# Kernel tuning notes

Measured on AMD Instinct MI355X. Metric: run time of the kernel, lower is better.

The kernel has to match this reference:

```python
import jax, jax.numpy as jnp
import numpy as np

N = 100000      # nodes
E = 1600000     # edges (avg degree 16)
F_IN = 64
HID = 128
OUT = 64


def setup_inputs() -> dict:
    key = jax.random.key(0)
    ks = jax.random.split(key, 12)
    s = lambda k, i, o: jax.random.normal(k, (i, o), jnp.float32) / np.sqrt(i)
    x = jax.random.normal(ks[0], (N, F_IN), jnp.float32)
    edge_index = jax.random.randint(ks[1], (2, E), 0, N, dtype=jnp.int64)
    return {
        "x": x,
        "edge_index": edge_index,
        # conv1: SAGEConv(F_IN -> HID): lin_l (neighbors, with bias), lin_r (root)
        "W1n": s(ks[2], F_IN, HID), "b1n": jnp.zeros((HID,), jnp.float32),
        "W1r": s(ks[3], F_IN, HID),
        # lin1: Linear(F_IN -> HID)
        "Wl1": s(ks[4], F_IN, HID), "bl1": jnp.zeros((HID,), jnp.float32),
        # conv2: SAGEConv(HID -> OUT)
        "W2n": s(ks[5], HID, OUT), "b2n": jnp.zeros((OUT,), jnp.float32),
        "W2r": s(ks[6], HID, OUT),
        # lin2: Linear(HID -> OUT)
        "Wl2": s(ks[7], HID, OUT), "bl2": jnp.zeros((OUT,), jnp.float32),
    }


def _sage(x, src, dst, Wn, bn, Wr):
    # mean aggregation of source-node features at destination nodes
    msg = x[src]                                             # [E, F]
    agg = jax.ops.segment_sum(msg, dst, num_segments=N)      # [N, F]
    deg = jax.ops.segment_sum(jnp.ones((src.shape[0],), x.dtype), dst,
                              num_segments=N)                # [N]
    mean = agg / jnp.maximum(deg, 1.0)[:, None]
    return mean @ Wn + bn + x @ Wr


def reference(x, edge_index, W1n, b1n, W1r, Wl1, bl1, W2n, b2n, W2r, Wl2, bl2):
    src, dst = edge_index[0], edge_index[1]
    h = _sage(x, src, dst, W1n, b1n, W1r) + (x @ Wl1 + bl1)
    h = jax.nn.relu(h)
    out = _sage(h, src, dst, W2n, b2n, W2r) + (h @ Wl2 + bl2)
    return out
```

## Files before the change

### kernel.cpp

```cpp
#include <hip/hip_runtime.h>


#define NN 100000
#define NE 1600000
#define SBW 256
#define NSB 391
#define CAP2 5120
#define EPB 6250
#define MB 256
#define BSB 256
#define W1B 32
#define W2B 32
#define XBLK ((NN * 8 + 511) / 512)

typedef __attribute__((ext_vector_type(8))) __bf16 bf16x8;
typedef __attribute__((ext_vector_type(4))) float f32x4;

__device__ __forceinline__ float b2f(unsigned short u) {
    unsigned v = ((unsigned)u) << 16;
    float f;
    __builtin_memcpy(&f, &v, 4);
    return f;
}
__device__ __forceinline__ float b2f_lo(unsigned v) {
    unsigned w = v << 16;
    float f;
    __builtin_memcpy(&f, &w, 4);
    return f;
}
__device__ __forceinline__ float b2f_hi(unsigned v) {
    unsigned w = v & 0xFFFF0000u;
    float f;
    __builtin_memcpy(&f, &w, 4);
    return f;
}
__device__ __forceinline__ unsigned short f2b(float f) {
    unsigned u;
    __builtin_memcpy(&u, &f, 4);
    u += 0x7FFFu + ((u >> 16) & 1u);
    return (unsigned short)(u >> 16);
}

__global__ __launch_bounds__(512) void front_kernel(
    const void* __restrict__ x, const int* __restrict__ ei,
    const void* W1n, const void* W1r, const void* Wl1,
    const void* b1n, const void* bl1,
    const void* W2n, const void* W2r, const void* Wl2,
    const void* b2n, const void* bl2,
    unsigned short* __restrict__ Wt1g, unsigned short* __restrict__ Wt2g,
    float* __restrict__ bias1, float* __restrict__ bias2,
    unsigned int* __restrict__ xbu,
    int* __restrict__ flags, int* __restrict__ cntP, int* __restrict__ ebuf) {
    __shared__ int lh[NSB];
    __shared__ int lbase[NSB];
    __shared__ int ldst[EPB];
    __shared__ int sred[256];
    int t = threadIdx.x;
    int b = blockIdx.x;

    if (b < BSB) {
        if (t < 256) sred[t] = ei[2 * t + 1];
        if (t < NSB) lh[t] = 0;
        __syncthreads();
        for (int s = 128; s > 0; s >>= 1) {
            if (t < s) sred[t] |= sred[t + s];
            __syncthreads();
        }
        bool i64 = (sred[0] == 0);
        int e0 = b * EPB;
        for (int i = t; i < EPB; i += 512) {
            int e = e0 + i;
            int d = i64 ? (int)((const long long*)ei)[NE + e] : ei[NE + e];
            ldst[i] = d;
            atomicAdd(&lh[d >> 8], 1);
        }
        __syncthreads();
        if (t < NSB) {
            int c = lh[t];
            lbase[t] = c ? atomicAdd(&cntP[t * 16], c) : 0;
            lh[t] = 0;
        }
        __syncthreads();
        for (int i = t; i < EPB; i += 512) {
            int e = e0 + i;
            int s = i64 ? (int)((const long long*)ei)[e] : ei[e];
            int d = ldst[i];
            int sb = d >> 8;
            int r = lbase[sb] + atomicAdd(&lh[sb], 1);
            if (r < CAP2) ebuf[sb * CAP2 + r] = (s << 8) | (d & 255);
        }
        return;
    }

    const unsigned int* xw = (const unsigned int*)x;
    if (t < 256) {
        unsigned e = (xw[t] >> 7) & 0xFFu;
        sred[t] = (e > 0x85u) ? 1 : 0;
    }
    __syncthreads();
    for (int s = 128; s > 0; s >>= 1) {
        if (t < s) sred[t] += sred[t + s];
        __syncthreads();
    }
    bool fp32 = sred[0] >= 32;
    auto rd = [&](const void* p, int i) -> float {
        return fp32 ? ((const float*)p)[i] : b2f(((const unsigned short*)p)[i]);
    };

    if (b < BSB + W1B) {
        int idx = (b - BSB) * 512 + t;
        int c = idx >> 7, k = idx & 127;
        float v = (k < 64) ? rd(W1n, k * 128 + c)
                           : rd(W1r, (k - 64) * 128 + c) + rd(Wl1, (k - 64) * 128 + c);
        Wt1g[c * 128 + k] = f2b(v);
        if (b == BSB) {
            if (t < 128) bias1[t] = rd(b1n, t) + rd(bl1, t);
            if (t == 0) flags[1] = fp32 ? 1 : 0;
        }
        return;
    }
    if (b < BSB + W1B + W2B) {
        int idx = (b - BSB - W1B) * 512 + t;
        int c = idx >> 7, k = idx & 127;
        float v = (c < 64) ? rd(W2n, k * 64 + c)
                           : rd(W2r, k * 64 + (c - 64)) + rd(Wl2, k * 64 + (c - 64));
        Wt2g[c * 128 + k] = f2b(v);
        if (b == BSB + W1B && t < 64) bias2[t] = rd(b2n, t) + rd(bl2, t);
        return;
    }
    int tt = (b - BSB - W1B - W2B) * 512 + t;
    if (tt >= NN * 8) return;
    if (fp32) {
        const float4* xf = (const float4*)x;
        float4 a = xf[2 * tt], c = xf[2 * tt + 1];
        uint4 o;
        o.x = f2b(a.x) | ((unsigned)f2b(a.y) << 16);
        o.y = f2b(a.z) | ((unsigned)f2b(a.w) << 16);
        o.z = f2b(c.x) | ((unsigned)f2b(c.y) << 16);
        o.w = f2b(c.z) | ((unsigned)f2b(c.w) << 16);
        ((uint4*)xbu)[tt] = o;
    } else {
        ((uint4*)xbu)[tt] = ((const uint4*)x)[tt];
    }
}

__global__ __launch_bounds__(512) void csr_build_kernel(
    const int* __restrict__ ebuf, const int* __restrict__ cntP,
    int* __restrict__ rpack, int* __restrict__ csr) {
    __shared__ int lcnt[SBW];
    __shared__ int lcur[SBW];
    int t = threadIdx.x, b = blockIdx.x;
    if (t < SBW) lcnt[t] = 0;
    __syncthreads();
    int base = b * CAP2;
    int cnt = min(cntP[b * 16], CAP2);
    for (int i = t; i < cnt; i += 512) atomicAdd(&lcnt[ebuf[base + i] & 255], 1);
    __syncthreads();
    int c = (t < SBW) ? lcnt[t] : 0;
    if (t < SBW) lcur[t] = c;
    __syncthreads();
    for (int off = 1; off < SBW; off <<= 1) {
        int add = 0;
        if (t < SBW && t >= off) add = lcur[t - off];
        __syncthreads();
        if (t < SBW) lcur[t] += add;
        __syncthreads();
    }
    if (t < SBW) {
        int excl = lcur[t] - c;
        int d0 = b * SBW + t;
        if (d0 < NN) rpack[d0] = ((base + excl) << 8) | min(c, 255);
        lcur[t] = excl;
    }
    __syncthreads();
    for (int i = t; i < cnt; i += 512) {
        int pk = ebuf[base + i];
        int r = atomicAdd(&lcur[pk & 255], 1);
        csr[base + r] = pk >> 8;
    }
}


__device__ __forceinline__ void gather_acc(
    const unsigned short* __restrict__ feat, const int* __restrict__ csr,
    int base, int deg, int fo, float* acc) {
    int t = 0;
    for (; t + 8 <= deg; t += 8) {
        int i0 = csr[base + t],     i1 = csr[base + t + 1];
        int i2 = csr[base + t + 2], i3 = csr[base + t + 3];
        int i4 = csr[base + t + 4], i5 = csr[base + t + 5];
        int i6 = csr[base + t + 6], i7 = csr[base + t + 7];
        bf16x8 v0 = *(const bf16x8*)(feat + (size_t)i0 * 64 + fo);
        bf16x8 v1 = *(const bf16x8*)(feat + (size_t)i1 * 64 + fo);
        bf16x8 v2 = *(const bf16x8*)(feat + (size_t)i2 * 64 + fo);
        bf16x8 v3 = *(const bf16x8*)(feat + (size_t)i3 * 64 + fo);
        bf16x8 v4 = *(const bf16x8*)(feat + (size_t)i4 * 64 + fo);
        bf16x8 v5 = *(const bf16x8*)(feat + (size_t)i5 * 64 + fo);
        bf16x8 v6 = *(const bf16x8*)(feat + (size_t)i6 * 64 + fo);
        bf16x8 v7 = *(const bf16x8*)(feat + (size_t)i7 * 64 + fo);
#pragma unroll
        for (int k = 0; k < 8; ++k)
            acc[k] += (((float)v0[k] + (float)v1[k]) + ((float)v2[k] + (float)v3[k]))
                    + (((float)v4[k] + (float)v5[k]) + ((float)v6[k] + (float)v7[k]));
    }
    for (; t + 4 <= deg; t += 4) {
        int i0 = csr[base + t],     i1 = csr[base + t + 1];
        int i2 = csr[base + t + 2], i3 = csr[base + t + 3];
        bf16x8 v0 = *(const bf16x8*)(feat + (size_t)i0 * 64 + fo);
        bf16x8 v1 = *(const bf16x8*)(feat + (size_t)i1 * 64 + fo);
        bf16x8 v2 = *(const bf16x8*)(feat + (size_t)i2 * 64 + fo);
        bf16x8 v3 = *(const bf16x8*)(feat + (size_t)i3 * 64 + fo);
#pragma unroll
        for (int k = 0; k < 8; ++k)
            acc[k] += ((float)v0[k] + (float)v1[k]) + ((float)v2[k] + (float)v3[k]);
    }
    for (; t < deg; ++t) {
        int i = csr[base + t];
        bf16x8 v = *(const bf16x8*)(feat + (size_t)i * 64 + fo);
#pragma unroll
        for (int k = 0; k < 8; ++k) acc[k] += (float)v[k];
    }
}

__global__ __launch_bounds__(256) void agg1_kernel(
    const unsigned short* __restrict__ feat, const int* __restrict__ rpack,
    const int* __restrict__ csr, unsigned int* __restrict__ mean1u) {
    int wid = threadIdx.x >> 6, lane = threadIdx.x & 63;
    int slot = lane >> 3, fo = (lane & 7) * 8;
    int d = (blockIdx.x * 4 + wid) * 8 + slot;
    int dd = min(d, NN - 1);
    int rp = rpack[dd];
    int base = rp >> 8;
    int deg = rp & 255;
    float acc[8];
#pragma unroll
    for (int k = 0; k < 8; ++k) acc[k] = 0.f;
    gather_acc(feat, csr, base, deg, fo, acc);
    if (d < NN) {
        float r = 1.0f / fmaxf((float)deg, 1.0f);
        uint4 o;
        o.x = f2b(acc[0] * r) | ((unsigned)f2b(acc[1] * r) << 16);
        o.y = f2b(acc[2] * r) | ((unsigned)f2b(acc[3] * r) << 16);
        o.z = f2b(acc[4] * r) | ((unsigned)f2b(acc[5] * r) << 16);
        o.w = f2b(acc[6] * r) | ((unsigned)f2b(acc[7] * r) << 16);
        *(uint4*)(mean1u + (size_t)d * 32 + (lane & 7) * 4) = o;
    }
}

__global__ __launch_bounds__(256) void agg2_kernel(
    const unsigned short* __restrict__ p, const int* __restrict__ rpack,
    const int* __restrict__ csr, const unsigned int* __restrict__ sfu,
    const float* __restrict__ bias2, const int* __restrict__ flags,
    void* __restrict__ out) {
    int wid = threadIdx.x >> 6, lane = threadIdx.x & 63;
    int slot = lane >> 3, fo = (lane & 7) * 8;
    int d = (blockIdx.x * 4 + wid) * 8 + slot;
    int dd = min(d, NN - 1);
    int rp = rpack[dd];
    int base = rp >> 8;
    int deg = rp & 255;
    float acc[8];
#pragma unroll
    for (int k = 0; k < 8; ++k) acc[k] = 0.f;
    gather_acc(p, csr, base, deg, fo, acc);
    if (d < NN) {
        float r = 1.0f / fmaxf((float)deg, 1.0f);
        uint4 sv = *(const uint4*)(sfu + (size_t)d * 32 + (lane & 7) * 4);
        float4 bA = *(const float4*)(bias2 + fo);
        float4 bB = *(const float4*)(bias2 + fo + 4);
        float v0 = acc[0] * r + b2f_lo(sv.x) + bA.x;
        float v1 = acc[1] * r + b2f_hi(sv.x) + bA.y;
        float v2 = acc[2] * r + b2f_lo(sv.y) + bA.z;
        float v3 = acc[3] * r + b2f_hi(sv.y) + bA.w;
        float v4 = acc[4] * r + b2f_lo(sv.z) + bB.x;
        float v5 = acc[5] * r + b2f_hi(sv.z) + bB.y;
        float v6 = acc[6] * r + b2f_lo(sv.w) + bB.z;
        float v7 = acc[7] * r + b2f_hi(sv.w) + bB.w;
        if (flags[1]) {
            float* op = (float*)out + (size_t)d * 64 + fo;
            *(float4*)op = make_float4(v0, v1, v2, v3);
            *(float4*)(op + 4) = make_float4(v4, v5, v6, v7);
        } else {
            uint4 o;
            o.x = f2b(v0) | ((unsigned)f2b(v1) << 16);
            o.y = f2b(v2) | ((unsigned)f2b(v3) << 16);
            o.z = f2b(v4) | ((unsigned)f2b(v5) << 16);
            o.w = f2b(v6) | ((unsigned)f2b(v7) << 16);
            *(uint4*)((unsigned int*)out + (size_t)d * 32 + (lane & 7) * 4) = o;
        }
    }
}

__global__ __launch_bounds__(512, 2) void gemmF_kernel(
    const unsigned short* __restrict__ mean1,
    const unsigned short* __restrict__ xb,
    const unsigned short* __restrict__ Wt1g, const float* __restrict__ bias1,
    const unsigned short* __restrict__ Wt2g,
    unsigned short* __restrict__ p, unsigned short* __restrict__ sf) {
    __shared__ unsigned short Wt1s[128 * 136];
    __shared__ unsigned short Wt2s[128 * 136];
    __shared__ unsigned short hs[MB * 136];
    int tid = threadIdx.x;
    int wid = tid >> 6, lane = tid & 63;
    int m = lane & 15, g = lane >> 4;
    int row0 = blockIdx.x * MB + wid * 32;

    bf16x8 a_frag[2][4];
#pragma unroll
    for (int t = 0; t < 2; ++t) {
        int arow = min(row0 + t * 16 + m, NN - 1);
#pragma unroll
        for (int kt = 0; kt < 4; ++kt) {
            int k0 = kt * 32 + g * 8;
            a_frag[t][kt] = (k0 < 64)
                ? *(const bf16x8*)(mean1 + (size_t)arow * 64 + k0)
                : *(const bf16x8*)(xb + (size_t)arow * 64 + (k0 - 64));
        }
    }

    for (int idx = tid; idx < 4096; idx += 512) {
        int c = (idx >> 4) & 127, ch = idx & 15;
        if (idx < 2048)
            *(bf16x8*)&Wt1s[c * 136 + ch * 8] = *(const bf16x8*)&Wt1g[c * 128 + ch * 8];
        else
            *(bf16x8*)&Wt2s[c * 136 + ch * 8] = *(const bf16x8*)&Wt2g[c * 128 + ch * 8];
    }
    __syncthreads();

    f32x4 acc[2][8];
#pragma unroll
    for (int t = 0; t < 2; ++t)
#pragma unroll
        for (int nt = 0; nt < 8; ++nt) acc[t][nt] = (f32x4){0.f, 0.f, 0.f, 0.f};

#pragma unroll
    for (int kt = 0; kt < 4; ++kt) {
        int k0 = kt * 32 + g * 8;
        bf16x8 b[8];
#pragma unroll
        for (int nt = 0; nt < 8; ++nt)
            b[nt] = *(const bf16x8*)(&Wt1s[(nt * 16 + m) * 136 + k0]);
#pragma unroll
        for (int nt = 0; nt < 8; ++nt) {
            acc[0][nt] = __builtin_amdgcn_mfma_f32_16x16x32_bf16(a_frag[0][kt], b[nt], acc[0][nt], 0, 0, 0);
            acc[1][nt] = __builtin_amdgcn_mfma_f32_16x16x32_bf16(a_frag[1][kt], b[nt], acc[1][nt], 0, 0, 0);
        }
    }

#pragma unroll
    for (int t = 0; t < 2; ++t)
#pragma unroll
        for (int nt = 0; nt < 8; ++nt) {
            int col = nt * 16 + m;
            float bias = bias1[col];
#pragma unroll
            for (int r = 0; r < 4; ++r) {
                float v = fmaxf(acc[t][nt][r] + bias, 0.0f);
                hs[(wid * 32 + t * 16 + g * 4 + r) * 136 + col] = f2b(v);
            }
        }

    bf16x8 a2[2][4];
#pragma unroll
    for (int t = 0; t < 2; ++t)
#pragma unroll
        for (int kt = 0; kt < 4; ++kt)
            a2[t][kt] = *(const bf16x8*)(&hs[(wid * 32 + t * 16 + m) * 136 + kt * 32 + g * 8]);

#pragma unroll
    for (int t = 0; t < 2; ++t)
#pragma unroll
        for (int nt = 0; nt < 8; ++nt) acc[t][nt] = (f32x4){0.f, 0.f, 0.f, 0.f};

#pragma unroll
    for (int kt = 0; kt < 4; ++kt) {
        int k0 = kt * 32 + g * 8;
        bf16x8 b[8];
#pragma unroll
        for (int nt = 0; nt < 8; ++nt)
            b[nt] = *(const bf16x8*)(&Wt2s[(nt * 16 + m) * 136 + k0]);
#pragma unroll
        for (int nt = 0; nt < 8; ++nt) {
            acc[0][nt] = __builtin_amdgcn_mfma_f32_16x16x32_bf16(a2[0][kt], b[nt], acc[0][nt], 0, 0, 0);
            acc[1][nt] = __builtin_amdgcn_mfma_f32_16x16x32_bf16(a2[1][kt], b[nt], acc[1][nt], 0, 0, 0);
        }
    }

#pragma unroll
    for (int t = 0; t < 2; ++t)
#pragma unroll
        for (int nt = 0; nt < 8; ++nt) {
            int col = nt * 16 + m;
#pragma unroll
            for (int r = 0; r < 4; ++r) {
                int row2 = row0 + t * 16 + g * 4 + r;
                if (row2 < NN) {
                    float v = acc[t][nt][r];
                    if (col < 64) p[(size_t)row2 * 64 + col] = f2b(v);
                    else          sf[(size_t)row2 * 64 + (col - 64)] = f2b(v);
                }
            }
        }
}

extern "C" void kernel_launch(void* const* d_in, const int* in_sizes, int n_in,
                              void* d_out, int out_size, void* d_ws, size_t ws_size,
                              hipStream_t stream) {
    const void* x   = d_in[0];
    const int*  ei  = (const int*)d_in[1];
    const void* W1n = d_in[2];
    const void* b1n = d_in[3];
    const void* W1r = d_in[4];
    const void* Wl1 = d_in[5];
    const void* bl1 = d_in[6];
    const void* W2n = d_in[7];
    const void* b2n = d_in[8];
    const void* W2r = d_in[9];
    const void* Wl2 = d_in[10];
    const void* bl2 = d_in[11];

    char* ws = (char*)d_ws;
    int*            flags = (int*)(ws + 0);
    int*            cntP  = (int*)(ws + 1024);
    float*          bias1 = (float*)(ws + 26112);
    float*          bias2 = (float*)(ws + 26624);
    unsigned short* Wt1g  = (unsigned short*)(ws + 26880);
    unsigned short* Wt2g  = (unsigned short*)(ws + 59648);
    int*            rpack = (int*)(ws + 92416);
    int*            csr   = (int*)(ws + 492544);
    unsigned short* xb    = (unsigned short*)(ws + 8500224);
    unsigned short* p     = xb;
    unsigned short* mean1 = (unsigned short*)(ws + 21300224);
    unsigned short* sf    = (unsigned short*)(ws + 34100224);
    int*            ebuf  = (int*)(ws + 46900224);

    (void)in_sizes; (void)n_in; (void)out_size; (void)ws_size;

    hipMemsetAsync(cntP, 0, NSB * 16 * sizeof(int), stream);
    front_kernel<<<BSB + W1B + W2B + XBLK, 512, 0, stream>>>(
        x, ei, W1n, W1r, Wl1, b1n, bl1, W2n, W2r, Wl2, b2n, bl2,
        Wt1g, Wt2g, bias1, bias2, (unsigned int*)xb, flags, cntP, ebuf);
    csr_build_kernel<<<NSB, 512, 0, stream>>>(ebuf, cntP, rpack, csr);
    agg1_kernel<<<(NN + 31) / 32, 256, 0, stream>>>(xb, rpack, csr, (unsigned int*)mean1);
    gemmF_kernel<<<(NN + MB - 1) / MB, 512, 0, stream>>>(mean1, xb, Wt1g, bias1, Wt2g, p, sf);
    agg2_kernel<<<(NN + 31) / 32, 256, 0, stream>>>(p, rpack, csr, (const unsigned int*)sf,
                                                    bias2, flags, d_out);
}
```

Measured before the change: 222.1 us.

## Sort destination nodes by degree within each bucket for balanced gather

```diff
diff --git a/kernel.cpp b/kernel.cpp
--- a/kernel.cpp
+++ b/kernel.cpp
@@ -5,6 +5,7 @@
 #define NE 1600000
 #define SBW 256
 #define NSB 391
+#define NSL (NSB * SBW)
 #define CAP2 5120
 #define EPB 6250
 #define MB 256
@@ -146,36 +147,56 @@
 
 __global__ __launch_bounds__(512) void csr_build_kernel(
     const int* __restrict__ ebuf, const int* __restrict__ cntP,
-    int* __restrict__ rpack, int* __restrict__ csr) {
+    int* __restrict__ spack, int* __restrict__ sidx, int* __restrict__ csr) {
     __shared__ int lcnt[SBW];
-    __shared__ int lcur[SBW];
+    __shared__ int lscan[SBW];
+    __shared__ int lstart[SBW];
+    __shared__ int dh[SBW];
     int t = threadIdx.x, b = blockIdx.x;
-    if (t < SBW) lcnt[t] = 0;
+    if (t < SBW) { lcnt[t] = 0; dh[t] = 0; }
     __syncthreads();
     int base = b * CAP2;
     int cnt = min(cntP[b * 16], CAP2);
     for (int i = t; i < cnt; i += 512) atomicAdd(&lcnt[ebuf[base + i] & 255], 1);
     __syncthreads();
-    int c = (t < SBW) ? lcnt[t] : 0;
-    if (t < SBW) lcur[t] = c;
+    int cc = (t < SBW) ? lcnt[t] : 0;
+    if (t < SBW) lscan[t] = cc;
     __syncthreads();
     for (int off = 1; off < SBW; off <<= 1) {
         int add = 0;
-        if (t < SBW && t >= off) add = lcur[t - off];
-        __syncthreads();
-        if (t < SBW) lcur[t] += add;
-        __syncthreads();
-    }
-    if (t < SBW) {
-        int excl = lcur[t] - c;
-        int d0 = b * SBW + t;
-        if (d0 < NN) rpack[d0] = ((base + excl) << 8) | min(c, 255);
-        lcur[t] = excl;
+        if (t < SBW && t >= off) add = lscan[t - off];
+        __syncthreads();
+        if (t < SBW) lscan[t] += add;
+        __syncthreads();
+    }
+    int d0 = b * SBW + t;
+    bool vld = (t < SBW) && (d0 < NN);
+    int dgc = min(cc, 255);
+    if (t < SBW) lstart[t] = lscan[t] - cc;
+    if (vld) atomicAdd(&dh[dgc], 1);
+    if (t < SBW) { spack[b * SBW + t] = 0; sidx[b * SBW + t] = -1; }
+    __syncthreads();
+    int hv = (t < SBW) ? dh[t] : 0;
+    if (t < SBW) lscan[t] = hv;
+    __syncthreads();
+    for (int off = 1; off < SBW; off <<= 1) {
+        int add = 0;
+        if (t < SBW && t >= off) add = lscan[t - off];
+        __syncthreads();
+        if (t < SBW) lscan[t] += add;
+        __syncthreads();
+    }
+    if (t < SBW) { dh[t] = lscan[t] - hv; lcnt[t] = 0; }
+    __syncthreads();
+    if (vld) {
+        int rank = dh[dgc] + atomicAdd(&lcnt[dgc], 1);
+        spack[b * SBW + rank] = ((base + lstart[t]) << 8) | dgc;
+        sidx[b * SBW + rank] = d0;
     }
     __syncthreads();
     for (int i = t; i < cnt; i += 512) {
         int pk = ebuf[base + i];
-        int r = atomicAdd(&lcur[pk & 255], 1);
+        int r = atomicAdd(&lstart[pk & 255], 1);
         csr[base + r] = pk >> 8;
     }
 }
@@ -223,49 +244,52 @@
 }
 
 __global__ __launch_bounds__(256) void agg1_kernel(
-    const unsigned short* __restrict__ feat, const int* __restrict__ rpack,
-    const int* __restrict__ csr, unsigned int* __restrict__ mean1u) {
+    const unsigned short* __restrict__ feat, const int* __restrict__ spack,
+    const int* __restrict__ sidx, const int* __restrict__ csr,
+    unsigned int* __restrict__ mean1u) {
     int wid = threadIdx.x >> 6, lane = threadIdx.x & 63;
     int slot = lane >> 3, fo = (lane & 7) * 8;
-    int d = (blockIdx.x * 4 + wid) * 8 + slot;
-    int dd = min(d, NN - 1);
-    int rp = rpack[dd];
+    int i = (blockIdx.x * 4 + wid) * 8 + slot;
+    int ii = min(i, NSL - 1);
+    int rp = spack[ii];
+    int sd = sidx[ii];
     int base = rp >> 8;
     int deg = rp & 255;
     float acc[8];
 #pragma unroll
     for (int k = 0; k < 8; ++k) acc[k] = 0.f;
     gather_acc(feat, csr, base, deg, fo, acc);
-    if (d < NN) {
+    if (i < NSL && sd >= 0) {
         float r = 1.0f / fmaxf((float)deg, 1.0f);
         uint4 o;
         o.x = f2b(acc[0] * r) | ((unsigned)f2b(acc[1] * r) << 16);
         o.y = f2b(acc[2] * r) | ((unsigned)f2b(acc[3] * r) << 16);
         o.z = f2b(acc[4] * r) | ((unsigned)f2b(acc[5] * r) << 16);
         o.w = f2b(acc[6] * r) | ((unsigned)f2b(acc[7] * r) << 16);
-        *(uint4*)(mean1u + (size_t)d * 32 + (lane & 7) * 4) = o;
+        *(uint4*)(mean1u + (size_t)sd * 32 + (lane & 7) * 4) = o;
     }
 }
 
 __global__ __launch_bounds__(256) void agg2_kernel(
-    const unsigned short* __restrict__ p, const int* __restrict__ rpack,
-    const int* __restrict__ csr, const unsigned int* __restrict__ sfu,
-    const float* __restrict__ bias2, const int* __restrict__ flags,
-    void* __restrict__ out) {
+    const unsigned short* __restrict__ p, const int* __restrict__ spack,
+    const int* __restrict__ sidx, const int* __restrict__ csr,
+    const unsigned int* __restrict__ sfu, const float* __restrict__ bias2,
+    const int* __restrict__ flags, void* __restrict__ out) {
     int wid = threadIdx.x >> 6, lane = threadIdx.x & 63;
     int slot = lane >> 3, fo = (lane & 7) * 8;
-    int d = (blockIdx.x * 4 + wid) * 8 + slot;
-    int dd = min(d, NN - 1);
-    int rp = rpack[dd];
+    int i = (blockIdx.x * 4 + wid) * 8 + slot;
+    int ii = min(i, NSL - 1);
+    int rp = spack[ii];
+    int sd = sidx[ii];
     int base = rp >> 8;
     int deg = rp & 255;
     float acc[8];
 #pragma unroll
     for (int k = 0; k < 8; ++k) acc[k] = 0.f;
     gather_acc(p, csr, base, deg, fo, acc);
-    if (d < NN) {
+    if (i < NSL && sd >= 0) {
         float r = 1.0f / fmaxf((float)deg, 1.0f);
-        uint4 sv = *(const uint4*)(sfu + (size_t)d * 32 + (lane & 7) * 4);
+        uint4 sv = *(const uint4*)(sfu + (size_t)sd * 32 + (lane & 7) * 4);
         float4 bA = *(const float4*)(bias2 + fo);
         float4 bB = *(const float4*)(bias2 + fo + 4);
         float v0 = acc[0] * r + b2f_lo(sv.x) + bA.x;
@@ -277,7 +301,7 @@
         float v6 = acc[6] * r + b2f_lo(sv.w) + bB.z;
         float v7 = acc[7] * r + b2f_hi(sv.w) + bB.w;
         if (flags[1]) {
-            float* op = (float*)out + (size_t)d * 64 + fo;
+            float* op = (float*)out + (size_t)sd * 64 + fo;
             *(float4*)op = make_float4(v0, v1, v2, v3);
             *(float4*)(op + 4) = make_float4(v4, v5, v6, v7);
         } else {
@@ -286,7 +310,7 @@
             o.y = f2b(v2) | ((unsigned)f2b(v3) << 16);
             o.z = f2b(v4) | ((unsigned)f2b(v5) << 16);
             o.w = f2b(v6) | ((unsigned)f2b(v7) << 16);
-            *(uint4*)((unsigned int*)out + (size_t)d * 32 + (lane & 7) * 4) = o;
+            *(uint4*)((unsigned int*)out + (size_t)sd * 32 + (lane & 7) * 4) = o;
         }
     }
 }
@@ -426,13 +450,14 @@
     float*          bias2 = (float*)(ws + 26624);
     unsigned short* Wt1g  = (unsigned short*)(ws + 26880);
     unsigned short* Wt2g  = (unsigned short*)(ws + 59648);
-    int*            rpack = (int*)(ws + 92416);
-    int*            csr   = (int*)(ws + 492544);
-    unsigned short* xb    = (unsigned short*)(ws + 8500224);
+    int*            spack = (int*)(ws + 92416);
+    int*            sidx  = (int*)(ws + 492800);
+    int*            csr   = (int*)(ws + 893184);
+    unsigned short* xb    = (unsigned short*)(ws + 8900864);
     unsigned short* p     = xb;
-    unsigned short* mean1 = (unsigned short*)(ws + 21300224);
-    unsigned short* sf    = (unsigned short*)(ws + 34100224);
-    int*            ebuf  = (int*)(ws + 46900224);
+    unsigned short* mean1 = (unsigned short*)(ws + 21700864);
+    unsigned short* sf    = (unsigned short*)(ws + 34500864);
+    int*            ebuf  = (int*)(ws + 47300864);
 
     (void)in_sizes; (void)n_in; (void)out_size; (void)ws_size;
 
@@ -440,9 +465,9 @@
     front_kernel<<<BSB + W1B + W2B + XBLK, 512, 0, stream>>>(
         x, ei, W1n, W1r, Wl1, b1n, bl1, W2n, W2r, Wl2, b2n, bl2,
         Wt1g, Wt2g, bias1, bias2, (unsigned int*)xb, flags, cntP, ebuf);
-    csr_build_kernel<<<NSB, 512, 0, stream>>>(ebuf, cntP, rpack, csr);
-    agg1_kernel<<<(NN + 31) / 32, 256, 0, stream>>>(xb, rpack, csr, (unsigned int*)mean1);
+    csr_build_kernel<<<NSB, 512, 0, stream>>>(ebuf, cntP, spack, sidx, csr);
+    agg1_kernel<<<NSL / 32, 256, 0, stream>>>(xb, spack, sidx, csr, (unsigned int*)mean1);
     gemmF_kernel<<<(NN + MB - 1) / MB, 512, 0, stream>>>(mean1, xb, Wt1g, bias1, Wt2g, p, sf);
-    agg2_kernel<<<(NN + 31) / 32, 256, 0, stream>>>(p, rpack, csr, (const unsigned int*)sf,
-                                                    bias2, flags, d_out);
-}
+    agg2_kernel<<<NSL / 32, 256, 0, stream>>>(p, spack, sidx, csr, (const unsigned int*)sf,
+                                              bias2, flags, d_out);
+}
```

Result: slower. 230.3 us (+3.7%).
